# Optimization experiments

Measured on AMD Instinct MI355X. Metric: run time of the kernel, lower is better.

Reference implementation:

```python
import jax, jax.numpy as jnp
import numpy as np

# --- static mask-construction config (mirrors FlexAttnFunc.init_mask args) ---
B = 1
L_F, L_H, L_W = 8, 20, 36      # latent_shape[2:]
A_F, A_H, A_W = 8, 1, 1        # action_shape[2:]
PATCH = (1, 2, 2)
CHUNK = 1
PAD = 176
WINDOW = 6
DIM, HEADS, DHEAD = 1536, 12, 128
EPS = 1e-5


def _make_ids():
    lf, lh, lw = L_F // PATCH[0], L_H // PATCH[1], L_W // PATCH[2]
    lat_seq = np.repeat(np.arange(B), lf * lh * lw)
    act_seq = np.repeat(np.arange(B), A_F * A_H * A_W)
    seq = np.concatenate([lat_seq, lat_seq, act_seq, act_seq])
    lat_fr = np.broadcast_to(np.arange(L_F)[None, :, None, None], (B, L_F, lh, lw)).reshape(-1)
    act_fr = np.broadcast_to(np.arange(A_F)[None, :, None, None], (B, A_F, A_H, A_W)).reshape(-1)
    fr = np.concatenate([lat_fr // CHUNK * 2] * 2 + [act_fr // CHUNK * 2 + 1] * 2)
    nz = np.concatenate([np.zeros_like(lat_fr), np.ones_like(lat_fr),
                         np.zeros_like(act_fr), np.ones_like(act_fr)])
    pad = np.full(PAD, -1, dtype=np.int64)
    return (np.concatenate([seq, pad]).astype(np.int32),
            np.concatenate([fr, pad]).astype(np.int32),
            np.concatenate([nz, pad]).astype(np.int32))


def setup_inputs() -> dict:
    key = jax.random.key(0)
    ks = jax.random.split(key, 8)
    seq, fr, nz = _make_ids()
    S = seq.shape[0]  # 3072
    sd = 0.02
    return {
        'x': jax.random.normal(ks[0], (1, S, DIM), jnp.float32),
        'Wq': jax.random.normal(ks[1], (DIM, DIM), jnp.float32) * sd,
        'bq': jnp.zeros((DIM,), jnp.float32),
        'Wk': jax.random.normal(ks[2], (DIM, DIM), jnp.float32) * sd,
        'bk': jnp.zeros((DIM,), jnp.float32),
        'Wv': jax.random.normal(ks[3], (DIM, DIM), jnp.float32) * sd,
        'bv': jnp.zeros((DIM,), jnp.float32),
        'gq': 1.0 + jax.random.normal(ks[4], (DIM,), jnp.float32) * sd,
        'gk': 1.0 + jax.random.normal(ks[5], (DIM,), jnp.float32) * sd,
        'Wo': jax.random.normal(ks[6], (DIM, DIM), jnp.float32) * sd,
        'bo': jnp.zeros((DIM,), jnp.float32),
        'seq_ids': jnp.asarray(seq),
        'frame_ids': jnp.asarray(fr),
        'noise_ids': jnp.asarray(nz),
        'window_size': WINDOW,
    }


def _rms(u, g):
    # torch.nn.RMSNorm over last dim (size heads*dim_head), elementwise affine
    return u * jax.lax.rsqrt(jnp.mean(u * u, axis=-1, keepdims=True) + EPS) * g


def _mask(seq_ids, frame_ids, noise_ids, window_size):
    sq, sk = seq_ids[:, None], seq_ids[None, :]
    fq, fk = frame_ids[:, None], frame_ids[None, :]
    nq, nk = noise_ids[:, None], noise_ids[None, :]
    seq_ok = (sq == sk) & (sq >= 0) & (sk >= 0)
    c2c = (nq == 1) & (nk == 1) & (fk <= fq)      # clean->clean, block causal incl self
    n2c = (nq == 0) & (nk == 1) & (fk < fq)       # noise->clean, causal excl self
    n2n = (nq == 0) & (nk == 0) & (fk == fq)      # noise->noise, same frame only
    win = jnp.abs(fq - fk) <= window_size
    return (c2c | n2c | n2n) & seq_ok & win


def reference(x, Wq, bq, Wk, bk, Wv, bv, gq, gk, Wo, bo,
              seq_ids, frame_ids, noise_ids, window_size):
    S = x.shape[1]
    q = _rms(x @ Wq + bq, gq)[0].reshape(S, HEADS, DHEAD)
    k = _rms(x @ Wk + bk, gk)[0].reshape(S, HEADS, DHEAD)
    v = (x @ Wv + bv)[0].reshape(S, HEADS, DHEAD)
    mask = _mask(seq_ids, frame_ids, noise_ids, window_size)  # [S,S] bool
    scores = jnp.einsum('qhd,khd->hqk', q, k) * (DHEAD ** -0.5)
    scores = jnp.where(mask[None], scores, jnp.float32(-1e9))
    attn = jax.nn.softmax(scores, axis=-1)
    o = jnp.einsum('hqk,khd->qhd', attn, v)
    # zero out padded (fully-masked) query rows
    o = o * (seq_ids >= 0).astype(o.dtype)[:, None, None]
    y = o.reshape(1, S, HEADS * DHEAD) @ Wo + bo
    return y
```

## Files before the change

### kernel.cpp

```cpp
#include <hip/hip_runtime.h>
#include <hip/hip_bf16.h>
#include <stdint.h>

typedef __bf16 bf16x8 __attribute__((ext_vector_type(8)));
typedef float f32x4 __attribute__((ext_vector_type(4)));

__device__ __forceinline__ unsigned short f2bf(float f) {
  union { float f; unsigned int u; } v; v.f = f;
  unsigned int u = v.u;
  unsigned int r = (u + 0x7fffu + ((u >> 16) & 1u)) >> 16;
  return (unsigned short)r;
}
__device__ __forceinline__ float bf2f(unsigned short s) {
  union { unsigned int u; float f; } v; v.u = ((unsigned int)s) << 16; return v.f;
}

__global__ __launch_bounds__(256) void setup(
    const float* __restrict__ x,
    const float* __restrict__ Wq, const float* __restrict__ Wk,
    const float* __restrict__ Wv, const float* __restrict__ Wo,
    const int* __restrict__ seq, const int* __restrict__ fr,
    const int* __restrict__ nz, const int* __restrict__ wsz,
    unsigned short* __restrict__ x_bf, unsigned short* __restrict__ wt,
    unsigned long long* __restrict__ tbm, unsigned char* __restrict__ mb,
    float* __restrict__ ssq, int S) {
  __shared__ __align__(16) unsigned char smu[16384];
  int b = blockIdx.x, tid = threadIdx.x;
  if (b < 1152) {
    int base = b * 1024 + tid;
    for (int j = 0; j < 4; j++) {
      int i = base + j * 256;
      float4 v = ((const float4*)x)[i];
      ushort4 o;
      o.x = f2bf(v.x); o.y = f2bf(v.y); o.z = f2bf(v.z); o.w = f2bf(v.w);
      ((ushort4*)x_bf)[i] = o;
    }
  } else if (b < 3456) {
    int id = b - 1152;
    int z = id / 576, rem = id % 576;
    int kx = rem % 24, ny = rem / 24;
    const float* W = z == 0 ? Wq : (z == 1 ? Wk : (z == 2 ? Wv : Wo));
    unsigned short (*t)[65] = (unsigned short(*)[65])smu;
    int k0 = kx * 64, n0 = ny * 64;
    const int N = 1536, K = 1536;
    for (int i = 0; i < 16; i++) {
      int e = tid + i * 256;
      int r = e >> 6, c = e & 63;
      t[r][c] = f2bf(W[(size_t)(k0 + r) * N + n0 + c]);
    }
    __syncthreads();
    for (int i = 0; i < 16; i++) {
      int e = tid + i * 256;
      int r = e >> 6, c = e & 63;
      wt[(size_t)(z * 1536 + n0 + r) * K + k0 + c] = t[c][r];
    }
  } else if (b == 3456) {
    int* ks_ = (int*)smu;
    unsigned int* tm_ = (unsigned int*)(smu + 12288);
    int W = wsz[0];
    for (int i = tid; i < S; i += 256) {
      int sq = seq[i];
      ks_[i] = (sq < 0) ? 0 : ((1 << 9) | ((nz[i] & 1) << 8) | (fr[i] & 15) | (sq << 10));
    }
    for (int i = tid; i < 6144; i += 256) ssq[i] = 0.f;
    __syncthreads();
    for (int t = tid; t < S / 32; t += 256) {
      unsigned int m = 0;
      for (int j = 0; j < 32; j++) {
        int a = ks_[t * 32 + j];
        if (a & (1 << 9)) m |= (a & (1 << 8)) ? (1u << (16 + (a & 15))) : (1u << (a & 15));
      }
      tm_[t] = m;
    }
    __syncthreads();
    for (int qg = tid; qg < S / 16; qg += 256) {
      unsigned int allowed = 0;
      for (int j = 0; j < 16; j++) {
        int a = ks_[qg * 16 + j];
        if (!(a & (1 << 9))) continue;
        int fq = a & 15, nq = (a >> 8) & 1;
        int lo = fq - W; if (lo < 0) lo = 0;
        unsigned int lom = ~((1u << lo) - 1);
        if (nq) allowed |= (((1u << (fq + 1)) - 1) & lom) << 16;
        else    allowed |= ((((1u << fq) - 1) & lom) << 16) | (1u << fq);
      }
      unsigned long long b0 = 0, b1 = 0;
      for (int t = 0; t < 96; t++)
        if (tm_[t] & allowed) { if (t < 64) b0 |= 1ull << t; else b1 |= 1ull << (t - 64); }
      tbm[qg * 2] = b0; tbm[qg * 2 + 1] = b1;
    }
  } else {
    int qg = b - 3457;
    int* ks_ = (int*)smu;
    int W = wsz[0];
    for (int i = tid; i < S; i += 256) {
      int sq = seq[i];
      ks_[i] = (sq < 0) ? 0 : ((1 << 9) | ((nz[i] & 1) << 8) | (fr[i] & 15) | (sq << 10));
    }
    __syncthreads();
    int wave = tid >> 6, lane = tid & 63, quad = lane >> 4, l16 = lane & 15;
    int aq[4];
    for (int r = 0; r < 4; r++) aq[r] = ks_[qg * 16 + quad * 4 + r];
    for (int t = wave; t < 96; t += 4) {
      int ak[2] = { ks_[t * 32 + l16], ks_[t * 32 + 16 + l16] };
      unsigned int byte = 0;
      for (int nt = 0; nt < 2; nt++) {
        int a = ak[nt];
        int kfr = a & 15, knz = (a >> 8) & 1, kvb = (a >> 9) & 1, ksq = a >> 10;
        for (int r = 0; r < 4; r++) {
          int bq_ = aq[r];
          int qfr = bq_ & 15, qnz = (bq_ >> 8) & 1, qvb = (bq_ >> 9) & 1, qsq = bq_ >> 10;
          bool ok  = qvb && kvb && (qsq == ksq);
          bool c2c = qnz && knz && (kfr <= qfr);
          bool n2c = !qnz && knz && (kfr < qfr);
          bool n2n = !qnz && !knz && (kfr == qfr);
          int df = qfr - kfr; df = df < 0 ? -df : df;
          if ((c2c || n2c || n2n) && ok && (df <= W)) byte |= 1u << (nt * 4 + r);
        }
      }
      mb[((size_t)qg * 96 + t) * 64 + lane] = (unsigned char)byte;
    }
  }
}

__global__ __launch_bounds__(256) void gemm_qkv(
    const unsigned short* __restrict__ A, const unsigned short* __restrict__ Bt,
    const float* __restrict__ bq, const float* __restrict__ bk, const float* __restrict__ bv,
    const float* __restrict__ gq, const float* __restrict__ gk,
    unsigned short* __restrict__ qt, unsigned short* __restrict__ ktb,
    unsigned short* __restrict__ vtb, float* __restrict__ ssq, int S) {
  const int K = 1536;
  __shared__ __align__(16) unsigned short smem[16384];
  unsigned short* As = smem;
  unsigned short* Bs = smem + 8192;
  unsigned short* Cs = smem;
  int tid = threadIdx.x, wave = tid >> 6, lane = tid & 63;
  int quad = lane >> 4, l16 = lane & 15;
  int m0 = blockIdx.x * 128, n0 = blockIdx.y * 128;
  int wm = (wave & 1) * 64, wn = (wave >> 1) * 64;
  int lr = lane >> 3;
  int lc = ((lane & 7) ^ lr) * 8;
  int sx = l16 & 7;
  f32x4 acc[4][4] = {};
  for (int k0 = 0; k0 < K; k0 += 64) {
    for (int c = 0; c < 4; c++) {
      int chunk = wave * 4 + c;
      int row = chunk * 8 + lr;
      const unsigned short* ga = &A[(size_t)(m0 + row) * K + k0 + lc];
      const unsigned short* gb = &Bt[(size_t)(n0 + row) * K + k0 + lc];
      __builtin_amdgcn_global_load_lds(
          (const __attribute__((address_space(1))) unsigned int*)ga,
          (__attribute__((address_space(3))) unsigned int*)(As + chunk * 512), 16, 0, 0);
      __builtin_amdgcn_global_load_lds(
          (const __attribute__((address_space(1))) unsigned int*)gb,
          (__attribute__((address_space(3))) unsigned int*)(Bs + chunk * 512), 16, 0, 0);
    }
    __syncthreads();
    for (int kk = 0; kk < 64; kk += 32) {
      int k8 = kk >> 3;
      int sw = ((k8 + quad) ^ sx) << 3;
      bf16x8 af[4], bfr[4];
      for (int i = 0; i < 4; i++)
        af[i] = *(const bf16x8*)&As[(wm + i * 16 + l16) * 64 + sw];
      for (int j = 0; j < 4; j++)
        bfr[j] = *(const bf16x8*)&Bs[(wn + j * 16 + l16) * 64 + sw];
      for (int i = 0; i < 4; i++)
        for (int j = 0; j < 4; j++)
          acc[i][j] = __builtin_amdgcn_mfma_f32_16x16x32_bf16(af[i], bfr[j], acc[i][j], 0, 0, 0);
    }
    __syncthreads();
  }
  int region = (n0 >= 3072) ? 2 : (n0 >= 1536 ? 1 : 0);
  int cbase = n0 - region * 1536;
  int hh = cbase >> 7;
  if (region < 2) {
    const float* bias = region == 0 ? bq : bk;
    float* ssqp = ssq + region * 3072;
    float ss[4][4] = {};
    for (int j = 0; j < 4; j++) {
      int col = cbase + wn + j * 16 + l16;
      float b = bias[col];
      float G = (region == 1) ? gq[col] * gk[col] : 1.0f;
      int cp = wn + j * 16 + l16;
      for (int i = 0; i < 4; i++)
        for (int r = 0; r < 4; r++) {
          float v = acc[i][j][r] + b;
          ss[i][r] += v * v;
          Cs[(wm + i * 16 + quad * 4 + r) * 128 + cp] = f2bf(v * G);
        }
    }
    for (int i = 0; i < 4; i++)
      for (int r = 0; r < 4; r++) {
        float v = ss[i][r];
        for (int o = 1; o < 16; o <<= 1) v += __shfl_xor(v, o);
        if (l16 == 0)
          atomicAdd(&ssqp[m0 + wm + i * 16 + quad * 4 + r], v);
      }
    __syncthreads();
    unsigned short* outp = (region == 0 ? qt : ktb) + (size_t)hh * 393216 + (size_t)m0 * 128;
    for (int p = 0; p < 8; p++) {
      int o = p * 2048 + tid * 8;
      *(uint4*)&outp[o] = *(const uint4*)&Cs[o];
    }
  } else {
    for (int j = 0; j < 4; j++) {
      int d = cbase + wn + j * 16 + l16;
      float b = bv[d];
      int cp = wn + j * 16 + l16;
      int c8 = l16 * 8;
      for (int i = 0; i < 4; i++)
        for (int r = 0; r < 4; r++) {
          int sp = wm + i * 16 + quad * 4 + r;
          Cs[cp * 128 + (sp ^ c8)] = f2bf(acc[i][j][r] + b);
        }
    }
    __syncthreads();
    unsigned short* outp = vtb + ((size_t)hh * 96 + (m0 >> 5)) * 4096;
    for (int p = 0; p < 8; p++) {
      int o = p * 2048 + tid * 8;
      int tile = o >> 12, rem = o & 4095;
      int dd = rem >> 5, s31 = rem & 31;
      int laddr = dd * 128 + ((tile * 32 + s31) ^ ((dd & 15) * 8));
      *(uint4*)&outp[o] = *(const uint4*)&Cs[laddr];
    }
  }
}

__global__ __launch_bounds__(256) void gemm_wo(
    const unsigned short* __restrict__ A, const unsigned short* __restrict__ Bt,
    const float* __restrict__ bias, float* __restrict__ C, int M, int N, int K) {
  __shared__ __align__(16) unsigned short As[128 * 64];
  __shared__ __align__(16) unsigned short Bs[64 * 64];
  int tid = threadIdx.x, wave = tid >> 6, lane = tid & 63;
  int quad = lane >> 4, l16 = lane & 15;
  int m0 = blockIdx.x * 128, n0 = blockIdx.y * 64;
  int wm = (wave & 1) * 64, wn = (wave >> 1) * 32;
  int lr = lane >> 3;
  int lc = ((lane & 7) ^ lr) * 8;
  int sx = l16 & 7;
  f32x4 acc[4][2] = {};
  for (int k0 = 0; k0 < K; k0 += 64) {
    for (int c = 0; c < 4; c++) {
      int chunk = wave * 4 + c;
      int row = chunk * 8 + lr;
      const unsigned short* ga = &A[(size_t)(m0 + row) * K + k0 + lc];
      __builtin_amdgcn_global_load_lds(
          (const __attribute__((address_space(1))) unsigned int*)ga,
          (__attribute__((address_space(3))) unsigned int*)(As + chunk * 512), 16, 0, 0);
    }
    for (int c = 0; c < 2; c++) {
      int chunk = wave * 2 + c;
      int row = chunk * 8 + lr;
      const unsigned short* gb = &Bt[(size_t)(n0 + row) * K + k0 + lc];
      __builtin_amdgcn_global_load_lds(
          (const __attribute__((address_space(1))) unsigned int*)gb,
          (__attribute__((address_space(3))) unsigned int*)(Bs + chunk * 512), 16, 0, 0);
    }
    __syncthreads();
    for (int kk = 0; kk < 64; kk += 32) {
      int k8 = kk >> 3;
      int sw = ((k8 + quad) ^ sx) << 3;
      bf16x8 af[4], bfr[2];
      for (int i = 0; i < 4; i++)
        af[i] = *(const bf16x8*)&As[(wm + i * 16 + l16) * 64 + sw];
      for (int j = 0; j < 2; j++)
        bfr[j] = *(const bf16x8*)&Bs[(wn + j * 16 + l16) * 64 + sw];
      for (int i = 0; i < 4; i++)
        for (int j = 0; j < 2; j++)
          acc[i][j] = __builtin_amdgcn_mfma_f32_16x16x32_bf16(af[i], bfr[j], acc[i][j], 0, 0, 0);
    }
    __syncthreads();
  }
  for (int j = 0; j < 2; j++) {
    int col = n0 + wn + j * 16 + l16;
    float b = bias[col];
    for (int i = 0; i < 4; i++)
      for (int r = 0; r < 4; r++)
        C[(size_t)(m0 + wm + i * 16 + quad * 4 + r) * N + col] = acc[i][j][r] + b;
  }
}

__global__ __launch_bounds__(256) void attn(
    const unsigned short* __restrict__ qt,
    const unsigned short* __restrict__ kt,
    const unsigned short* __restrict__ vt,
    const unsigned char* __restrict__ mb,
    const unsigned long long* __restrict__ tbm,
    const float* __restrict__ ssq,
    unsigned short* __restrict__ op0b, unsigned short* __restrict__ op1b,
    float* __restrict__ lp, int S) {
  const int h = blockIdx.x;
  const int qb64 = blockIdx.y;
  const int split = blockIdx.z;
  int tid = threadIdx.x, wave = tid >> 6, lane = tid & 63;
  int quad = lane >> 4, l16 = lane & 15;
  const float scale = 0.088388347648318447f;

  __shared__ __align__(16) unsigned short Ks[2][4096];
  __shared__ __align__(16) unsigned short Vs[2][4096];
  __shared__ __align__(16) unsigned short pshare[4][16][40];

  int qg = qb64 * 4 + wave;
  unsigned long long bm0 = tbm[(qb64 * 4) * 2]     | tbm[(qb64 * 4 + 1) * 2] |
                           tbm[(qb64 * 4 + 2) * 2] | tbm[(qb64 * 4 + 3) * 2];
  unsigned long long bm1 = tbm[(qb64 * 4) * 2 + 1]     | tbm[(qb64 * 4 + 1) * 2 + 1] |
                           tbm[(qb64 * 4 + 2) * 2 + 1] | tbm[(qb64 * 4 + 3) * 2 + 1];
  unsigned long long wb0 = tbm[qg * 2], wb1 = tbm[qg * 2 + 1];

  const unsigned short* kth = kt + (size_t)h * 96 * 4096;
  const unsigned short* vth = vt + (size_t)h * 96 * 4096;
  const unsigned char* mbq = mb + (size_t)qg * 96 * 64;

  bf16x8 qf[4];
  {
    const unsigned short* qp = qt + ((size_t)(h * 192 + qg) * 16 + l16) * 128 + quad * 8;
    for (int ks = 0; ks < 4; ks++) qf[ks] = *(const bf16x8*)&qp[ks * 32];
  }
  float qs[4];
  for (int r = 0; r < 4; r++) {
    int row = qb64 * 64 + wave * 16 + quad * 4 + r;
    qs[r] = rsqrtf(ssq[row] * (1.0f / 1536.0f) + 1e-5f) * scale;
  }
  const float* ssk = ssq + 3072;

  f32x4 oacc[8] = {};
  f32x4 lacc = {};
  const __bf16 onebf = (__bf16)1.0f;
  const bf16x8 ones = {onebf, onebf, onebf, onebf, onebf, onebf, onebf, onebf};

#define POP(dst) do { \
    if (bm0) { dst = __builtin_ctzll(bm0); bm0 &= bm0 - 1; } \
    else if (bm1) { dst = 64 + __builtin_ctzll(bm1); bm1 &= bm1 - 1; } \
    else dst = -1; } while (0)

#define STAGE(t_, b_) do { \
    for (int j = 0; j < 2; j++) { \
      int slot = j * 256 + tid; \
      int key = slot >> 4, cc = slot & 15; \
      const unsigned short* src = kth + (size_t)(t_) * 4096 + key * 128 + (cc ^ (key & 15)) * 8; \
      __builtin_amdgcn_global_load_lds( \
          (const __attribute__((address_space(1))) unsigned int*)src, \
          (__attribute__((address_space(3))) unsigned int*)(&Ks[b_][0] + j * 2048 + wave * 512), \
          16, 0, 0); \
    } \
    for (int j = 0; j < 2; j++) { \
      int slot = j * 256 + tid; \
      int row = slot >> 2, cc = slot & 3; \
      const unsigned short* src = vth + (size_t)(t_) * 4096 + row * 32 + (cc ^ ((row >> 1) & 3)) * 8; \
      __builtin_amdgcn_global_load_lds( \
          (const __attribute__((address_space(1))) unsigned int*)src, \
          (__attribute__((address_space(3))) unsigned int*)(&Vs[b_][0] + j * 2048 + wave * 512), \
          16, 0, 0); \
    } } while (0)

  int t, dsc;
  if (split) POP(dsc);
  POP(t);
  unsigned int mbyte = 0;
  float kss0 = 0.f, kss1 = 0.f;
  if (t >= 0) {
    STAGE(t, 0);
    mbyte = mbq[t * 64 + lane];
    kss0 = ssk[t * 32 + l16]; kss1 = ssk[t * 32 + 16 + l16];
  }
  __syncthreads();
  int buf = 0;

  while (t >= 0) {
    POP(dsc);
    int tn; POP(tn);
    unsigned int mbyte2 = 0;
    float nss0 = 0.f, nss1 = 0.f;
    if (tn >= 0) {
      STAGE(tn, buf ^ 1);
      mbyte2 = mbq[tn * 64 + lane];
      nss0 = ssk[tn * 32 + l16]; nss1 = ssk[tn * 32 + 16 + l16];
    }

    bool live = (t < 64) ? ((wb0 >> t) & 1) : ((wb1 >> (t - 64)) & 1);
    if (live) {
      f32x4 sacc[2] = {};
      for (int nt = 0; nt < 2; nt++) {
        int key = nt * 16 + l16;
        for (int ks = 0; ks < 4; ks++) {
          int cc = (ks * 4 + quad) ^ l16;
          bf16x8 kf = *(const bf16x8*)&Ks[buf][(key * 16 + cc) * 8];
          sacc[nt] = __builtin_amdgcn_mfma_f32_16x16x32_bf16(qf[ks], kf, sacc[nt], 0, 0, 0);
        }
      }
      float ksc[2];
      ksc[0] = rsqrtf(kss0 * (1.0f / 1536.0f) + 1e-5f);
      ksc[1] = rsqrtf(kss1 * (1.0f / 1536.0f) + 1e-5f);
      for (int nt = 0; nt < 2; nt++)
        for (int r = 0; r < 4; r++) {
          float e = __expf(sacc[nt][r] * (qs[r] * ksc[nt]) - 16.0f);
          float p = ((mbyte >> (nt * 4 + r)) & 1) ? e : 0.0f;
          pshare[wave][quad * 4 + r][nt * 16 + l16] = f2bf(p);
        }
      __asm__ __volatile__("s_waitcnt lgkmcnt(0)" ::: "memory");
      bf16x8 pf = *(const bf16x8*)&pshare[wave][l16][quad * 8];
      for (int d = 0; d < 8; d++) {
        int row = d * 16 + l16;
        int cc = quad ^ ((l16 >> 1) & 3);
        bf16x8 vf = *(const bf16x8*)&Vs[buf][(row * 4 + cc) * 8];
        oacc[d] = __builtin_amdgcn_mfma_f32_16x16x32_bf16(pf, vf, oacc[d], 0, 0, 0);
      }
      lacc = __builtin_amdgcn_mfma_f32_16x16x32_bf16(pf, ones, lacc, 0, 0, 0);
    }
    __syncthreads();
    buf ^= 1;
    t = tn;
    mbyte = mbyte2;
    kss0 = nss0; kss1 = nss1;
  }
#undef POP
#undef STAGE

  unsigned short* po = split ? op1b : op0b;
  for (int r = 0; r < 4; r++) {
    int q = qb64 * 64 + wave * 16 + quad * 4 + r;
    float inv = (lacc[r] > 0.f) ? 1.0f / lacc[r] : 0.0f;
    for (int d = 0; d < 8; d++)
      po[((size_t)h * S + q) * 128 + d * 16 + l16] = f2bf(oacc[d][r] * inv);
    if (l16 == 0)
      lp[((size_t)split * 12 + h) * S + q] = lacc[r];
  }
}

__global__ __launch_bounds__(256) void combine(const unsigned short* __restrict__ op0b,
                                               const unsigned short* __restrict__ op1b,
                                               const float* __restrict__ lp,
                                               const int* __restrict__ seq,
                                               unsigned short* __restrict__ ob, int S) {
  int e4 = blockIdx.x * 256 + threadIdx.x;
  int idx = e4 * 4;
  int per_h = S * 128;
  int h = idx / per_h;
  int rem = idx - h * per_h;
  int q = rem >> 7, dd = rem & 127;
  float l0 = lp[(size_t)h * S + q], l1 = lp[(size_t)(12 + h) * S + q];
  float tot = l0 + l1;
  float ok = (seq[q] >= 0 && tot > 0.f) ? 1.0f / tot : 0.0f;
  float w0 = l0 * ok, w1 = l1 * ok;
  ushort4 a = ((const ushort4*)op0b)[e4];
  ushort4 b = ((const ushort4*)op1b)[e4];
  ushort4 o;
  o.x = f2bf(bf2f(a.x) * w0 + bf2f(b.x) * w1);
  o.y = f2bf(bf2f(a.y) * w0 + bf2f(b.y) * w1);
  o.z = f2bf(bf2f(a.z) * w0 + bf2f(b.z) * w1);
  o.w = f2bf(bf2f(a.w) * w0 + bf2f(b.w) * w1);
  *(ushort4*)&ob[(size_t)q * 1536 + h * 128 + dd] = o;
}

extern "C" void kernel_launch(void* const* d_in, const int* in_sizes, int n_in,
                              void* d_out, int out_size, void* d_ws, size_t ws_size,
                              hipStream_t stream) {
  const float* x  = (const float*)d_in[0];
  const float* Wq = (const float*)d_in[1];
  const float* bq = (const float*)d_in[2];
  const float* Wk = (const float*)d_in[3];
  const float* bk = (const float*)d_in[4];
  const float* Wv = (const float*)d_in[5];
  const float* bv = (const float*)d_in[6];
  const float* gq = (const float*)d_in[7];
  const float* gk = (const float*)d_in[8];
  const float* Wo = (const float*)d_in[9];
  const float* bo = (const float*)d_in[10];
  const int* seq  = (const int*)d_in[11];
  const int* fr   = (const int*)d_in[12];
  const int* nz   = (const int*)d_in[13];
  const int* wsz  = (const int*)d_in[14];
  float* out = (float*)d_out;
  const int S = in_sizes[11];
  const int D = 1536;

  char* ws = (char*)d_ws;
  size_t off = 0;
  unsigned short* x_bf = (unsigned short*)(ws + off); off += (size_t)S * D * 2;
  unsigned short* wt   = (unsigned short*)(ws + off); off += (size_t)4 * D * D * 2;
  unsigned short* qt   = (unsigned short*)(ws + off); off += (size_t)S * D * 2;
  unsigned short* ktb  = (unsigned short*)(ws + off); off += (size_t)S * D * 2;
  unsigned short* vtb  = (unsigned short*)(ws + off); off += (size_t)S * D * 2;
  unsigned short* o_bf = (unsigned short*)(ws + off); off += (size_t)S * D * 2;
  unsigned short* op0b = (unsigned short*)(ws + off); off += (size_t)S * D * 2;
  unsigned short* op1b = (unsigned short*)(ws + off); off += (size_t)S * D * 2;
  unsigned long long* tbm = (unsigned long long*)(ws + off); off += (size_t)(S / 16) * 16;
  unsigned char*  mbuf = (unsigned char*)(ws + off);  off += (size_t)(S / 16) * 96 * 64;
  float*          lp   = (float*)(ws + off);          off += (size_t)2 * 12 * S * 4;
  float*          ssq  = (float*)(ws + off);          off += (size_t)2 * 3072 * 4;

  dim3 blk(256);
  setup<<<dim3(3649), blk, 0, stream>>>(x, Wq, Wk, Wv, Wo, seq, fr, nz, wsz,
                                        x_bf, wt, tbm, mbuf, ssq, S);
  gemm_qkv<<<dim3(S / 128, 3 * D / 128), blk, 0, stream>>>(x_bf, wt, bq, bk, bv, gq, gk,
                                                           qt, ktb, vtb, ssq, S);
  attn<<<dim3(D / 128, S / 64, 2), blk, 0, stream>>>(qt, ktb, vtb, mbuf, tbm, ssq,
                                                     op0b, op1b, lp, S);
  combine<<<dim3(12 * S * 128 / 4 / 256), blk, 0, stream>>>(op0b, op1b, lp, seq, o_bf, S);
  gemm_wo<<<dim3(S / 128, D / 64), blk, 0, stream>>>(o_bf, wt + (size_t)3 * D * D,
                                                     bo, out, S, D, D);
}
```

Measured before the change: 288.7 us.

## Rewrite QKV GEMM with 256x256 tiles, 512 threads and double-buffered LDS pipeline

The QKV projection GEMM moves from 128x128 tiles with 4 waves to 256x256 tiles with 8 waves. It uses a double-buffered 128KB LDS stage: global-to-LDS loads for the next k-tile are split into quarters and issued between MFMA phases, with manual waitcnt, barriers and setprio. The aim is to raise data reuse per tile and hide global load latency behind MFMA work. The cost is fewer blocks (12x18=216 on a 256-CU part), one block per CU because of the LDS size, and more complex synchronisation. The epilogue is adapted so each block writes two heads.

```diff
diff --git a/kernel.cpp b/kernel.cpp
--- a/kernel.cpp
+++ b/kernel.cpp
@@ -123,105 +123,140 @@
   }
 }
 
-__global__ __launch_bounds__(256) void gemm_qkv(
+__global__ __launch_bounds__(512) void gemm_qkv(
     const unsigned short* __restrict__ A, const unsigned short* __restrict__ Bt,
     const float* __restrict__ bq, const float* __restrict__ bk, const float* __restrict__ bv,
     const float* __restrict__ gq, const float* __restrict__ gk,
     unsigned short* __restrict__ qt, unsigned short* __restrict__ ktb,
     unsigned short* __restrict__ vtb, float* __restrict__ ssq, int S) {
-  const int K = 1536;
-  __shared__ __align__(16) unsigned short smem[16384];
-  unsigned short* As = smem;
-  unsigned short* Bs = smem + 8192;
-  unsigned short* Cs = smem;
-  int tid = threadIdx.x, wave = tid >> 6, lane = tid & 63;
+  __shared__ __align__(16) unsigned short smem[65536];
+  int tid = threadIdx.x, wid = tid >> 6, lane = tid & 63;
   int quad = lane >> 4, l16 = lane & 15;
-  int m0 = blockIdx.x * 128, n0 = blockIdx.y * 128;
-  int wm = (wave & 1) * 64, wn = (wave >> 1) * 64;
+  int m0 = blockIdx.x * 256, n0 = blockIdx.y * 256;
+  int wm = (wid >> 2) * 128;
+  int wn = (wid & 3) * 64;
   int lr = lane >> 3;
-  int lc = ((lane & 7) ^ lr) * 8;
+  int lsw = ((lane & 7) ^ lr) * 8;
   int sx = l16 & 7;
-  f32x4 acc[4][4] = {};
-  for (int k0 = 0; k0 < K; k0 += 64) {
-    for (int c = 0; c < 4; c++) {
-      int chunk = wave * 4 + c;
-      int row = chunk * 8 + lr;
-      const unsigned short* ga = &A[(size_t)(m0 + row) * K + k0 + lc];
-      const unsigned short* gb = &Bt[(size_t)(n0 + row) * K + k0 + lc];
-      __builtin_amdgcn_global_load_lds(
-          (const __attribute__((address_space(1))) unsigned int*)ga,
-          (__attribute__((address_space(3))) unsigned int*)(As + chunk * 512), 16, 0, 0);
-      __builtin_amdgcn_global_load_lds(
-          (const __attribute__((address_space(1))) unsigned int*)gb,
-          (__attribute__((address_space(3))) unsigned int*)(Bs + chunk * 512), 16, 0, 0);
-    }
-    __syncthreads();
-    for (int kk = 0; kk < 64; kk += 32) {
-      int k8 = kk >> 3;
-      int sw = ((k8 + quad) ^ sx) << 3;
-      bf16x8 af[4], bfr[4];
-      for (int i = 0; i < 4; i++)
-        af[i] = *(const bf16x8*)&As[(wm + i * 16 + l16) * 64 + sw];
-      for (int j = 0; j < 4; j++)
-        bfr[j] = *(const bf16x8*)&Bs[(wn + j * 16 + l16) * 64 + sw];
-      for (int i = 0; i < 4; i++)
-        for (int j = 0; j < 4; j++)
-          acc[i][j] = __builtin_amdgcn_mfma_f32_16x16x32_bf16(af[i], bfr[j], acc[i][j], 0, 0, 0);
-    }
-    __syncthreads();
-  }
+
+  f32x4 acc[8][4] = {};
+
+#define STAGEQ(t_, q_) do { \
+    if ((t_) < 24) { \
+      int b_ = (t_) & 1; \
+      int k0_ = (t_) * 64; \
+      unsigned short* ldsb = ((q_) < 2) ? (smem + b_ * 16384) : (smem + 32768 + b_ * 16384); \
+      const unsigned short* gsrc = ((q_) < 2) ? A : Bt; \
+      int rbase = ((q_) < 2) ? m0 : n0; \
+      int lo8_ = ((q_) & 1) * 8; \
+      for (int c_ = 0; c_ < 2; c_++) { \
+        int chunk = lo8_ + c_ * 16 + wid; \
+        const unsigned short* src = gsrc + (size_t)(rbase + chunk * 8 + lr) * 1536 + k0_ + lsw; \
+        __builtin_amdgcn_global_load_lds( \
+            (const __attribute__((address_space(1))) unsigned int*)src, \
+            (__attribute__((address_space(3))) unsigned int*)(ldsb + chunk * 512 + lane * 8), 16, 0, 0); \
+      } \
+    } } while (0)
+
+  STAGEQ(0, 0); STAGEQ(0, 1); STAGEQ(0, 2); STAGEQ(0, 3);
+  STAGEQ(1, 0);
+  asm volatile("s_waitcnt vmcnt(2)" ::: "memory");
+  __builtin_amdgcn_s_barrier();
+  __builtin_amdgcn_sched_barrier(0);
+
+#define PHASE(p) do { \
+    constexpr int q_ = (p) & 3; \
+    constexpr int tb_ = (p) >> 2; \
+    constexpr int k8_ = (q_ >> 1) * 4; \
+    constexpr int mi0_ = (q_ & 1) * 4; \
+    unsigned short* Ab = smem + tb_ * 16384; \
+    unsigned short* Bb = smem + 32768 + tb_ * 16384; \
+    int so_ = ((k8_ + quad) ^ sx) << 3; \
+    if constexpr ((q_ & 1) == 0) { \
+      for (int nj = 0; nj < 4; nj++) \
+        bfr[nj] = *(const bf16x8*)&Bb[(wn + nj * 16 + l16) * 64 + so_]; \
+    } \
+    bf16x8 af[4]; \
+    for (int ii = 0; ii < 4; ii++) \
+      af[ii] = *(const bf16x8*)&Ab[(wm + (mi0_ + ii) * 16 + l16) * 64 + so_]; \
+    STAGEQ(2 * i + kStT[p], kStQ[p]); \
+    __builtin_amdgcn_sched_barrier(0); \
+    __builtin_amdgcn_s_setprio(1); \
+    for (int ii = 0; ii < 4; ii++) \
+      for (int nj = 0; nj < 4; nj++) \
+        acc[mi0_ + ii][nj] = __builtin_amdgcn_mfma_f32_16x16x32_bf16(af[ii], bfr[nj], acc[mi0_ + ii][nj], 0, 0, 0); \
+    __builtin_amdgcn_s_setprio(0); \
+    if constexpr (q_ == 3) { asm volatile("s_waitcnt vmcnt(2)" ::: "memory"); } \
+    __builtin_amdgcn_s_barrier(); \
+    __builtin_amdgcn_sched_barrier(0); \
+  } while (0)
+
+  constexpr int kStT[8] = {1, 1, 1, 2, 2, 2, 2, 3};
+  constexpr int kStQ[8] = {1, 2, 3, 0, 1, 2, 3, 0};
+
+  for (int i = 0; i < 12; i++) {
+    bf16x8 bfr[4];
+    PHASE(0); PHASE(1); PHASE(2); PHASE(3);
+    PHASE(4); PHASE(5); PHASE(6); PHASE(7);
+  }
+#undef PHASE
+#undef STAGEQ
+
   int region = (n0 >= 3072) ? 2 : (n0 >= 1536 ? 1 : 0);
   int cbase = n0 - region * 1536;
-  int hh = cbase >> 7;
+  int hh0 = cbase >> 7;
+  unsigned short* Cs = smem;
   if (region < 2) {
     const float* bias = region == 0 ? bq : bk;
     float* ssqp = ssq + region * 3072;
-    float ss[4][4] = {};
-    for (int j = 0; j < 4; j++) {
-      int col = cbase + wn + j * 16 + l16;
-      float b = bias[col];
-      float G = (region == 1) ? gq[col] * gk[col] : 1.0f;
-      int cp = wn + j * 16 + l16;
-      for (int i = 0; i < 4; i++)
+    float ss[8][4] = {};
+    for (int nj = 0; nj < 4; nj++) {
+      int col = wn + nj * 16 + l16;
+      float b = bias[cbase + col];
+      float G = (region == 1) ? gq[cbase + col] * gk[cbase + col] : 1.0f;
+      for (int mi = 0; mi < 8; mi++)
         for (int r = 0; r < 4; r++) {
-          float v = acc[i][j][r] + b;
-          ss[i][r] += v * v;
-          Cs[(wm + i * 16 + quad * 4 + r) * 128 + cp] = f2bf(v * G);
+          float v = acc[mi][nj][r] + b;
+          ss[mi][r] += v * v;
+          Cs[(wm + mi * 16 + quad * 4 + r) * 256 + col] = f2bf(v * G);
         }
     }
-    for (int i = 0; i < 4; i++)
+    for (int mi = 0; mi < 8; mi++)
       for (int r = 0; r < 4; r++) {
-        float v = ss[i][r];
+        float v = ss[mi][r];
         for (int o = 1; o < 16; o <<= 1) v += __shfl_xor(v, o);
         if (l16 == 0)
-          atomicAdd(&ssqp[m0 + wm + i * 16 + quad * 4 + r], v);
-      }
-    __syncthreads();
-    unsigned short* outp = (region == 0 ? qt : ktb) + (size_t)hh * 393216 + (size_t)m0 * 128;
-    for (int p = 0; p < 8; p++) {
-      int o = p * 2048 + tid * 8;
-      *(uint4*)&outp[o] = *(const uint4*)&Cs[o];
+          atomicAdd(&ssqp[m0 + wm + mi * 16 + quad * 4 + r], v);
+      }
+    __syncthreads();
+    unsigned short* outb = (region == 0 ? qt : ktb);
+    for (int p = 0; p < 16; p++) {
+      int o = p * 4096 + tid * 8;
+      int row = o >> 8, col = o & 255;
+      size_t dst = (size_t)(hh0 + (col >> 7)) * 393216 + (size_t)(m0 + row) * 128 + (col & 127);
+      *(uint4*)&outb[dst] = *(const uint4*)&Cs[o];
     }
   } else {
-    for (int j = 0; j < 4; j++) {
-      int d = cbase + wn + j * 16 + l16;
-      float b = bv[d];
-      int cp = wn + j * 16 + l16;
+    for (int nj = 0; nj < 4; nj++) {
+      int col = wn + nj * 16 + l16;
+      float b = bv[cbase + col];
       int c8 = l16 * 8;
-      for (int i = 0; i < 4; i++)
+      for (int mi = 0; mi < 8; mi++)
         for (int r = 0; r < 4; r++) {
-          int sp = wm + i * 16 + quad * 4 + r;
-          Cs[cp * 128 + (sp ^ c8)] = f2bf(acc[i][j][r] + b);
+          int sp = wm + mi * 16 + quad * 4 + r;
+          Cs[col * 256 + (sp ^ c8)] = f2bf(acc[mi][nj][r] + b);
         }
     }
     __syncthreads();
-    unsigned short* outp = vtb + ((size_t)hh * 96 + (m0 >> 5)) * 4096;
-    for (int p = 0; p < 8; p++) {
-      int o = p * 2048 + tid * 8;
-      int tile = o >> 12, rem = o & 4095;
-      int dd = rem >> 5, s31 = rem & 31;
-      int laddr = dd * 128 + ((tile * 32 + s31) ^ ((dd & 15) * 8));
-      *(uint4*)&outp[o] = *(const uint4*)&Cs[laddr];
+    for (int hh = 0; hh < 2; hh++) {
+      unsigned short* outp = vtb + ((size_t)(hh0 + hh) * 96 + (m0 >> 5)) * 4096;
+      for (int p = 0; p < 8; p++) {
+        int o = p * 4096 + tid * 8;
+        int tile = o >> 12, rem = o & 4095;
+        int dd = rem >> 5, s31 = rem & 31;
+        int laddr = (hh * 128 + dd) * 256 + ((tile * 32 + s31) ^ ((dd & 15) * 8));
+        *(uint4*)&outp[o] = *(const uint4*)&Cs[laddr];
+      }
     }
   }
 }
@@ -492,8 +527,8 @@
   dim3 blk(256);
   setup<<<dim3(3649), blk, 0, stream>>>(x, Wq, Wk, Wv, Wo, seq, fr, nz, wsz,
                                         x_bf, wt, tbm, mbuf, ssq, S);
-  gemm_qkv<<<dim3(S / 128, 3 * D / 128), blk, 0, stream>>>(x_bf, wt, bq, bk, bv, gq, gk,
-                                                           qt, ktb, vtb, ssq, S);
+  gemm_qkv<<<dim3(S / 256, 3 * D / 256), dim3(512), 0, stream>>>(x_bf, wt, bq, bk, bv, gq, gk,
+                                                                 qt, ktb, vtb, ssq, S);
   attn<<<dim3(D / 128, S / 64, 2), blk, 0, stream>>>(qt, ktb, vtb, mbuf, tbm, ssq,
                                                      op0b, op1b, lp, S);
   combine<<<dim3(12 * S * 128 / 4 / 256), blk, 0, stream>>>(op0b, op1b, lp, seq, o_bf, S);
```

After: 270.3 us. 1.07x faster.
